# Kernel tuning notes

Measured on AMD Instinct MI355X. Metric: run time of the kernel, lower is better.

## Reference

```python
import jax, jax.numpy as jnp
import numpy as np

D_MODEL = 1024
NUM_HEADS = 16
D_K = D_MODEL // NUM_HEADS
B, T = 2, 2048


def setup_inputs() -> dict:
    key = jax.random.key(0)
    ks = jax.random.split(key, 9)
    s = 1.0 / np.sqrt(D_MODEL)
    inp = {"x": jax.random.normal(ks[0], (B, T, D_MODEL), dtype=jnp.float32)}
    for i, name in enumerate(["q", "k", "v", "out"]):
        inp[f"W_{name}"] = jax.random.uniform(ks[1 + 2 * i], (D_MODEL, D_MODEL), jnp.float32, -s, s)
        inp[f"b_{name}"] = jax.random.uniform(ks[2 + 2 * i], (D_MODEL,), jnp.float32, -s, s)
    return inp


def reference(x, W_q, b_q, W_k, b_k, W_v, b_v, W_out, b_out):
    b, t, _ = x.shape
    # torch Linear: y = x @ W.T + b
    def proj(inp, W, bias):
        y = inp @ W.T + bias
        return y.reshape(b, -1, NUM_HEADS, D_K).transpose(0, 2, 1, 3)  # [B,H,T,d_k]

    Q = proj(x, W_q, b_q)
    K = proj(x, W_k, b_k)
    V = proj(x, W_v, b_v)
    scores = jnp.einsum("bhqd,bhkd->bhqk", Q, K) / jnp.sqrt(jnp.float32(D_K))
    attn = jax.nn.softmax(scores, axis=-1)
    ctx = jnp.einsum("bhqk,bhkd->bhqd", attn, V)
    ctx = ctx.transpose(0, 2, 1, 3).reshape(b, t, D_MODEL)
    return ctx @ W_out.T + b_out
```

## Files before the change

### kernel.cpp

```cpp
#include <hip/hip_runtime.h>
#include <hip/hip_bf16.h>

typedef __attribute__((ext_vector_type(8))) short short8;
typedef __attribute__((ext_vector_type(4))) short short4v;
typedef __attribute__((ext_vector_type(4))) float floatx4;

__device__ __forceinline__ unsigned short f2b(float f) {
  unsigned int v;
  __builtin_memcpy(&v, &f, 4);
  unsigned int r = (v + 0x7FFFu + ((v >> 16) & 1u)) >> 16;
  return (unsigned short)r;
}

__device__ __forceinline__ unsigned int f2b_pk(float a, float b) {
  unsigned int ua, ub;
  __builtin_memcpy(&ua, &a, 4);
  __builtin_memcpy(&ub, &b, 4);
  ua = ua + 0x7FFFu + ((ua >> 16) & 1u);
  ub = ub + 0x7FFFu + ((ub >> 16) & 1u);
#if __has_builtin(__builtin_amdgcn_perm)
  return __builtin_amdgcn_perm(ub, ua, 0x07060302u);
#else
  return (ub & 0xFFFF0000u) | (ua >> 16);
#endif
}

__device__ __forceinline__ float fast_exp2(float x) {
#if __has_builtin(__builtin_amdgcn_exp2f)
  return __builtin_amdgcn_exp2f(x);
#else
  return __builtin_exp2f(x);
#endif
}

__device__ __forceinline__ void async_copy16(const void* g, void* l) {
  __builtin_amdgcn_global_load_lds(
      (const __attribute__((address_space(1))) unsigned int*)g,
      (__attribute__((address_space(3))) unsigned int*)l, 16, 0, 0);
}

#define QSCALE 0.18033688011112042f

__global__ __launch_bounds__(256) void cvt_all_kernel(
    const float* __restrict__ x,
    const float* __restrict__ w0, const float* __restrict__ w1,
    const float* __restrict__ w2, const float* __restrict__ w3,
    unsigned short* __restrict__ xb,
    unsigned short* __restrict__ d0, unsigned short* __restrict__ d1,
    unsigned short* __restrict__ d2, unsigned short* __restrict__ d3)
{
  int gid = blockIdx.x * 256 + threadIdx.x;
  const float* src;
  unsigned short* dst;
  size_t off;
  if (gid < (1 << 20)) {
    src = x; dst = xb; off = gid;
  } else {
    int g = gid - (1 << 20);
    int w = g >> 18;
    off = g & 0x3FFFF;
    src = (w == 0) ? w0 : (w == 1) ? w1 : (w == 2) ? w2 : w3;
    dst = (w == 0) ? d0 : (w == 1) ? d1 : (w == 2) ? d2 : d3;
  }
  floatx4 v = *(const floatx4*)(src + off * 4);
  unsigned int lo = f2b_pk(v[0], v[1]), hi = f2b_pk(v[2], v[3]);
  unsigned long long r = ((unsigned long long)hi << 32) | lo;
  *(unsigned long long*)(dst + off * 4) = r;
}

__global__ __launch_bounds__(256) void gemm_qkv_kernel(
    const unsigned short* __restrict__ A,
    const unsigned short* __restrict__ W0, const unsigned short* __restrict__ W1,
    const unsigned short* __restrict__ W2,
    const float* __restrict__ bias0, const float* __restrict__ bias1,
    const float* __restrict__ bias2,
    unsigned short* __restrict__ Qo, unsigned short* __restrict__ Ko,
    unsigned short* __restrict__ VTo)
{
  const int z = blockIdx.z;
  const unsigned short* W  = (z == 0) ? W0 : (z == 1) ? W1 : W2;
  const float* bias        = (z == 0) ? bias0 : (z == 1) ? bias1 : bias2;

  __shared__ alignas(16) unsigned short sA[128 * 32];
  __shared__ alignas(16) unsigned short sB[128 * 32];

  const int tid  = threadIdx.x;
  const int lane = tid & 63;
  const int wave = tid >> 6;
  const int col  = lane & 15;
  const int quad = lane >> 4;
  const int wm   = (wave >> 1) * 64;
  const int wn   = (wave & 1) * 64;
  const int m0   = blockIdx.y * 128;
  const int n0   = blockIdx.x * 128;
  const int swz8 = (quad ^ ((col >> 1) & 3)) * 8;

  floatx4 acc[4][4];
#pragma unroll
  for (int i = 0; i < 4; ++i)
#pragma unroll
    for (int j = 0; j < 4; ++j) acc[i][j] = (floatx4){0.f, 0.f, 0.f, 0.f};

  for (int k0 = 0; k0 < 1024; k0 += 32) {
    __syncthreads();
#pragma unroll
    for (int i = 0; i < 2; ++i) {
      int c   = i * 256 + tid;
      int row = c >> 2;
      int cs  = (c & 3) ^ ((c >> 3) & 3);
      int ko  = cs * 8;
      async_copy16(A + (size_t)(m0 + row) * 1024 + k0 + ko, sA + c * 8);
      async_copy16(W + (size_t)(n0 + row) * 1024 + k0 + ko, sB + c * 8);
    }
    __syncthreads();
    short8 af[4], bf[4];
#pragma unroll
    for (int mi = 0; mi < 4; ++mi)
      af[mi] = *(const short8*)(sA + (wm + mi * 16 + col) * 32 + swz8);
#pragma unroll
    for (int ni = 0; ni < 4; ++ni)
      bf[ni] = *(const short8*)(sB + (wn + ni * 16 + col) * 32 + swz8);
#pragma unroll
    for (int mi = 0; mi < 4; ++mi)
#pragma unroll
      for (int ni = 0; ni < 4; ++ni)
        acc[mi][ni] = __builtin_amdgcn_mfma_f32_16x16x32_bf16(af[mi], bf[ni], acc[mi][ni], 0, 0, 0);
  }

#pragma unroll
  for (int ni = 0; ni < 4; ++ni) {
    int n = n0 + wn + ni * 16 + col;
    float bv = bias[n];
#pragma unroll
    for (int mi = 0; mi < 4; ++mi) {
      int mbase = m0 + wm + mi * 16 + quad * 4;
      if (z == 2) {
        int d = n & 63, h = n >> 6;
        int bb = mbase >> 11, t = mbase & 2047;
        unsigned int lo = f2b_pk(acc[mi][ni][0] + bv, acc[mi][ni][1] + bv);
        unsigned int hi = f2b_pk(acc[mi][ni][2] + bv, acc[mi][ni][3] + bv);
        unsigned long long wv = ((unsigned long long)hi << 32) | lo;
        *(unsigned long long*)(VTo + (((size_t)bb * 16 + h) * 64 + d) * 2048 + t) = wv;
      } else {
#pragma unroll
        for (int r = 0; r < 4; ++r) {
          int m = mbase + r;
          float val = acc[mi][ni][r] + bv;
          if (z == 0) Qo[(size_t)m * 1024 + n] = f2b(val * QSCALE);
          else        Ko[(size_t)m * 1024 + n] = f2b(val);
        }
      }
    }
  }
}

__global__ __launch_bounds__(256) void gemm_out_kernel(
    const unsigned short* __restrict__ A, const unsigned short* __restrict__ W,
    const float* __restrict__ bias, float* __restrict__ DF)
{
  __shared__ alignas(16) unsigned short sA[128 * 32];
  __shared__ alignas(16) unsigned short sB[64 * 32];

  const int tid  = threadIdx.x;
  const int lane = tid & 63;
  const int wave = tid >> 6;
  const int col  = lane & 15;
  const int quad = lane >> 4;
  const int wm   = (wave >> 1) * 64;
  const int wn   = (wave & 1) * 32;
  const int m0   = blockIdx.y * 128;
  const int n0   = blockIdx.x * 64;
  const int swz8 = (quad ^ ((col >> 1) & 3)) * 8;

  floatx4 acc[4][2];
#pragma unroll
  for (int i = 0; i < 4; ++i)
#pragma unroll
    for (int j = 0; j < 2; ++j) acc[i][j] = (floatx4){0.f, 0.f, 0.f, 0.f};

  for (int k0 = 0; k0 < 1024; k0 += 32) {
    __syncthreads();
#pragma unroll
    for (int i = 0; i < 2; ++i) {
      int c   = i * 256 + tid;
      int row = c >> 2;
      int cs  = (c & 3) ^ ((c >> 3) & 3);
      async_copy16(A + (size_t)(m0 + row) * 1024 + k0 + cs * 8, sA + c * 8);
    }
    {
      int row = tid >> 2;
      int cs  = (tid & 3) ^ ((tid >> 3) & 3);
      async_copy16(W + (size_t)(n0 + row) * 1024 + k0 + cs * 8, sB + tid * 8);
    }
    __syncthreads();
    short8 af[4], bf[2];
#pragma unroll
    for (int mi = 0; mi < 4; ++mi)
      af[mi] = *(const short8*)(sA + (wm + mi * 16 + col) * 32 + swz8);
#pragma unroll
    for (int ni = 0; ni < 2; ++ni)
      bf[ni] = *(const short8*)(sB + (wn + ni * 16 + col) * 32 + swz8);
#pragma unroll
    for (int mi = 0; mi < 4; ++mi)
#pragma unroll
      for (int ni = 0; ni < 2; ++ni)
        acc[mi][ni] = __builtin_amdgcn_mfma_f32_16x16x32_bf16(af[mi], bf[ni], acc[mi][ni], 0, 0, 0);
  }

#pragma unroll
  for (int ni = 0; ni < 2; ++ni) {
    int n = n0 + wn + ni * 16 + col;
    float bv = bias[n];
#pragma unroll
    for (int mi = 0; mi < 4; ++mi) {
      int mbase = m0 + wm + mi * 16 + quad * 4;
#pragma unroll
      for (int r = 0; r < 4; ++r)
        DF[(size_t)(mbase + r) * 1024 + n] = acc[mi][ni][r] + bv;
    }
  }
}

__global__ __launch_bounds__(256, 2) void attention_kernel(
    const unsigned short* __restrict__ Q, const unsigned short* __restrict__ K,
    const unsigned short* __restrict__ VT, unsigned short* __restrict__ CTX)
{
  __shared__ alignas(16) unsigned short sK[2][8192];
  __shared__ alignas(16) unsigned short sV[2][8192];
  __shared__ alignas(16) unsigned short sP[4][32 * 64];

  const int flat = blockIdx.x;
  const int idx  = flat >> 3;
  const int bh   = (flat & 7) * 4 + (idx >> 4);
  const int q0   = (idx & 15) * 128;
  const int b = bh >> 4, h = bh & 15;

  const int tid  = threadIdx.x;
  const int lane = tid & 63;
  const int wave = tid >> 6;
  const int col  = lane & 15;
  const int quad = lane >> 4;
  const int c7   = col & 7;
  const int swz8 = (quad ^ ((col >> 1) & 3)) * 8;

  const int srow = tid >> 2;
  const int sko  = ((tid & 3) ^ ((tid >> 3) & 3)) * 8;

  const unsigned short* kbase = K + ((size_t)b * 2048 + srow) * 1024 + h * 64;
  const unsigned short* vbase = VT + ((size_t)bh * 64 + srow) * 2048;

  short8 qfA[2], qfB[2];
  {
    const unsigned short* qp =
        Q + ((size_t)(b * 2048 + q0 + wave * 32 + col)) * 1024 + h * 64 + quad * 8;
    qfA[0] = *(const short8*)qp;
    qfA[1] = *(const short8*)(qp + 32);
    qfB[0] = *(const short8*)(qp + 16 * 1024);
    qfB[1] = *(const short8*)(qp + 16 * 1024 + 32);
  }

#define STAGE_KV128(ktv, buf)                                                  \
  do {                                                                         \
    _Pragma("unroll")                                                          \
    for (int kh = 0; kh < 2; ++kh) {                                           \
      _Pragma("unroll")                                                        \
      for (int i = 0; i < 2; ++i) {                                            \
        async_copy16(kbase + (size_t)((ktv) + kh * 64) * 1024 + i * 32 + sko,  \
                     sK[buf] + kh * 4096 + (i * 256 + tid) * 8);               \
        async_copy16(vbase + (ktv) + kh * 64 + i * 32 + sko,                   \
                     sV[buf] + kh * 4096 + (i * 256 + tid) * 8);               \
      }                                                                        \
    }                                                                          \
  } while (0)

  STAGE_KV128(0, 0);

  floatx4 OA[4], OB[4];
#pragma unroll
  for (int f = 0; f < 4; ++f) {
    OA[f] = (floatx4){0.f, 0.f, 0.f, 0.f};
    OB[f] = (floatx4){0.f, 0.f, 0.f, 0.f};
  }
  float laccA = 0.f, laccB = 0.f;

  unsigned short* myP = &sP[wave][0];

  for (int kt = 0; kt < 2048; kt += 128) {
    const int cur = (kt >> 7) & 1;
    __syncthreads();
    if (kt + 128 < 2048) {
      STAGE_KV128(kt + 128, cur ^ 1);
    }

#pragma unroll
    for (int kh = 0; kh < 2; ++kh) {
      const unsigned short* sKc = sK[cur] + kh * 4096;
      const unsigned short* sVc = sV[cur] + kh * 4096;

      floatx4 STA[4], STB[4];
      __builtin_amdgcn_s_setprio(1);
#pragma unroll
      for (int f = 0; f < 4; ++f) {
        short8 kf0 = *(const short8*)(sKc + (f * 16 + col) * 32 + swz8);
        short8 kf1 = *(const short8*)(sKc + 2048 + (f * 16 + col) * 32 + swz8);
        STA[f] = (floatx4){0.f, 0.f, 0.f, 0.f};
        STA[f] = __builtin_amdgcn_mfma_f32_16x16x32_bf16(kf0, qfA[0], STA[f], 0, 0, 0);
        STA[f] = __builtin_amdgcn_mfma_f32_16x16x32_bf16(kf1, qfA[1], STA[f], 0, 0, 0);
        STB[f] = (floatx4){0.f, 0.f, 0.f, 0.f};
        STB[f] = __builtin_amdgcn_mfma_f32_16x16x32_bf16(kf0, qfB[0], STB[f], 0, 0, 0);
        STB[f] = __builtin_amdgcn_mfma_f32_16x16x32_bf16(kf1, qfB[1], STB[f], 0, 0, 0);
      }
      __builtin_amdgcn_s_setprio(0);

#pragma unroll
      for (int f = 0; f < 4; ++f) {
        float a0 = fast_exp2(STA[f][0]);
        float a1 = fast_exp2(STA[f][1]);
        float a2 = fast_exp2(STA[f][2]);
        float a3 = fast_exp2(STA[f][3]);
        laccA += (a0 + a1) + (a2 + a3);
        unsigned long long wA =
            ((unsigned long long)f2b_pk(a2, a3) << 32) | f2b_pk(a0, a1);
        *(unsigned long long*)(myP + col * 64 +
                               (((f * 2 + (quad >> 1)) ^ c7) * 8) + (quad & 1) * 4) = wA;
        float b0 = fast_exp2(STB[f][0]);
        float b1 = fast_exp2(STB[f][1]);
        float b2 = fast_exp2(STB[f][2]);
        float b3 = fast_exp2(STB[f][3]);
        laccB += (b0 + b1) + (b2 + b3);
        unsigned long long wB =
            ((unsigned long long)f2b_pk(b2, b3) << 32) | f2b_pk(b0, b1);
        *(unsigned long long*)(myP + (16 + col) * 64 +
                               (((f * 2 + (quad >> 1)) ^ c7) * 8) + (quad & 1) * 4) = wB;
      }

      short8 pfA0 = *(const short8*)(myP + col * 64 + ((quad ^ c7) * 8));
      short8 pfA1 = *(const short8*)(myP + col * 64 + (((quad + 4) ^ c7) * 8));
      short8 pfB0 = *(const short8*)(myP + (16 + col) * 64 + ((quad ^ c7) * 8));
      short8 pfB1 = *(const short8*)(myP + (16 + col) * 64 + (((quad + 4) ^ c7) * 8));
      __builtin_amdgcn_s_setprio(1);
#pragma unroll
      for (int f = 0; f < 4; ++f) {
        short8 vf0 = *(const short8*)(sVc + (f * 16 + col) * 32 + swz8);
        short8 vf1 = *(const short8*)(sVc + 2048 + (f * 16 + col) * 32 + swz8);
        OA[f] = __builtin_amdgcn_mfma_f32_16x16x32_bf16(pfA0, vf0, OA[f], 0, 0, 0);
        OA[f] = __builtin_amdgcn_mfma_f32_16x16x32_bf16(pfA1, vf1, OA[f], 0, 0, 0);
        OB[f] = __builtin_amdgcn_mfma_f32_16x16x32_bf16(pfB0, vf0, OB[f], 0, 0, 0);
        OB[f] = __builtin_amdgcn_mfma_f32_16x16x32_bf16(pfB1, vf1, OB[f], 0, 0, 0);
      }
      __builtin_amdgcn_s_setprio(0);
    }
  }

  laccA += __shfl_xor(laccA, 16, 64);
  laccA += __shfl_xor(laccA, 32, 64);
  laccB += __shfl_xor(laccB, 16, 64);
  laccB += __shfl_xor(laccB, 32, 64);
  float invA[4], invB[4];
#pragma unroll
  for (int r = 0; r < 4; ++r) {
    invA[r] = 1.f / __shfl(laccA, quad * 4 + r, 16);
    invB[r] = 1.f / __shfl(laccB, quad * 4 + r, 16);
  }

#pragma unroll
  for (int f = 0; f < 4; ++f) {
#pragma unroll
    for (int r = 0; r < 4; ++r) {
      int qA = q0 + wave * 32 + quad * 4 + r;
      int d = f * 16 + col;
      CTX[(size_t)(b * 2048 + qA) * 1024 + h * 64 + d] = f2b(OA[f][r] * invA[r]);
      CTX[(size_t)(b * 2048 + qA + 16) * 1024 + h * 64 + d] = f2b(OB[f][r] * invB[r]);
    }
  }
}

extern "C" void kernel_launch(void* const* d_in, const int* in_sizes, int n_in,
                              void* d_out, int out_size, void* d_ws, size_t ws_size,
                              hipStream_t stream) {
  const float* x   = (const float*)d_in[0];
  const float* W_q = (const float*)d_in[1];
  const float* b_q = (const float*)d_in[2];
  const float* W_k = (const float*)d_in[3];
  const float* b_k = (const float*)d_in[4];
  const float* W_v = (const float*)d_in[5];
  const float* b_v = (const float*)d_in[6];
  const float* W_o = (const float*)d_in[7];
  const float* b_o = (const float*)d_in[8];
  float* out = (float*)d_out;

  const size_t NX = (size_t)4096 * 1024;
  const size_t NW = (size_t)1024 * 1024;

  unsigned short* p   = (unsigned short*)d_ws;
  unsigned short* xb  = p;  p += NX;
  unsigned short* Wqb = p;  p += NW;
  unsigned short* Wkb = p;  p += NW;
  unsigned short* Wvb = p;  p += NW;
  unsigned short* Wob = p;  p += NW;
  unsigned short* Q   = p;  p += NX;
  unsigned short* Kb  = p;  p += NX;
  unsigned short* VT  = p;  p += NX;
  unsigned short* CTX = p;  p += NX;

  dim3 blk(256);
  cvt_all_kernel<<<dim3(8192), blk, 0, stream>>>(
      x, W_q, W_k, W_v, W_o, xb, Wqb, Wkb, Wvb, Wob);
  gemm_qkv_kernel<<<dim3(8, 32, 3), blk, 0, stream>>>(
      xb, Wqb, Wkb, Wvb, b_q, b_k, b_v, Q, Kb, VT);
  attention_kernel<<<dim3(512), blk, 0, stream>>>(Q, Kb, VT, CTX);
  gemm_out_kernel<<<dim3(16, 32), blk, 0, stream>>>(CTX, Wob, b_o, out);
}
```

Baseline: 192.7 us.

## Double per-wave query rows in attention to raise K/V tile reuse

Each attention block now handles 256 query rows instead of 128, with each wave processing 64 rows (four 16-row groups) against each staged K/V tile. This halves the number of blocks and the total K/V traffic from global to shared memory per query. The cost is higher register pressure (launch bounds dropped to one block per SM), a larger P scratch area in shared memory, and only 256 blocks on a 256-CU device, so there is less latency hiding.

```diff
diff --git a/kernel.cpp b/kernel.cpp
--- a/kernel.cpp
+++ b/kernel.cpp
@@ -221,18 +221,18 @@
   }
 }
 
-__global__ __launch_bounds__(256, 2) void attention_kernel(
+__global__ __launch_bounds__(256, 1) void attention_kernel(
     const unsigned short* __restrict__ Q, const unsigned short* __restrict__ K,
     const unsigned short* __restrict__ VT, unsigned short* __restrict__ CTX)
 {
   __shared__ alignas(16) unsigned short sK[2][8192];
   __shared__ alignas(16) unsigned short sV[2][8192];
-  __shared__ alignas(16) unsigned short sP[4][32 * 64];
+  __shared__ alignas(16) unsigned short sP[4][64 * 64];
 
   const int flat = blockIdx.x;
   const int idx  = flat >> 3;
-  const int bh   = (flat & 7) * 4 + (idx >> 4);
-  const int q0   = (idx & 15) * 128;
+  const int bh   = (flat & 7) * 4 + (idx >> 3);
+  const int q0   = (idx & 7) * 256;
   const int b = bh >> 4, h = bh & 15;
 
   const int tid  = threadIdx.x;
@@ -249,14 +249,15 @@
   const unsigned short* kbase = K + ((size_t)b * 2048 + srow) * 1024 + h * 64;
   const unsigned short* vbase = VT + ((size_t)bh * 64 + srow) * 2048;
 
-  short8 qfA[2], qfB[2];
+  short8 qf[4][2];
   {
     const unsigned short* qp =
-        Q + ((size_t)(b * 2048 + q0 + wave * 32 + col)) * 1024 + h * 64 + quad * 8;
-    qfA[0] = *(const short8*)qp;
-    qfA[1] = *(const short8*)(qp + 32);
-    qfB[0] = *(const short8*)(qp + 16 * 1024);
-    qfB[1] = *(const short8*)(qp + 16 * 1024 + 32);
+        Q + ((size_t)(b * 2048 + q0 + wave * 64 + col)) * 1024 + h * 64 + quad * 8;
+#pragma unroll
+    for (int g = 0; g < 4; ++g) {
+      qf[g][0] = *(const short8*)(qp + (size_t)g * 16 * 1024);
+      qf[g][1] = *(const short8*)(qp + (size_t)g * 16 * 1024 + 32);
+    }
   }
 
 #define STAGE_KV128(ktv, buf)                                                  \
@@ -275,13 +276,12 @@
 
   STAGE_KV128(0, 0);
 
-  floatx4 OA[4], OB[4];
-#pragma unroll
-  for (int f = 0; f < 4; ++f) {
-    OA[f] = (floatx4){0.f, 0.f, 0.f, 0.f};
-    OB[f] = (floatx4){0.f, 0.f, 0.f, 0.f};
-  }
-  float laccA = 0.f, laccB = 0.f;
+  floatx4 O[4][4];
+#pragma unroll
+  for (int g = 0; g < 4; ++g)
+#pragma unroll
+    for (int f = 0; f < 4; ++f) O[g][f] = (floatx4){0.f, 0.f, 0.f, 0.f};
+  float lacc[4] = {0.f, 0.f, 0.f, 0.f};
 
   unsigned short* myP = &sP[wave][0];
 
@@ -297,80 +297,80 @@
       const unsigned short* sKc = sK[cur] + kh * 4096;
       const unsigned short* sVc = sV[cur] + kh * 4096;
 
-      floatx4 STA[4], STB[4];
+      floatx4 ST[4][4];
       __builtin_amdgcn_s_setprio(1);
 #pragma unroll
       for (int f = 0; f < 4; ++f) {
         short8 kf0 = *(const short8*)(sKc + (f * 16 + col) * 32 + swz8);
         short8 kf1 = *(const short8*)(sKc + 2048 + (f * 16 + col) * 32 + swz8);
-        STA[f] = (floatx4){0.f, 0.f, 0.f, 0.f};
-        STA[f] = __builtin_amdgcn_mfma_f32_16x16x32_bf16(kf0, qfA[0], STA[f], 0, 0, 0);
-        STA[f] = __builtin_amdgcn_mfma_f32_16x16x32_bf16(kf1, qfA[1], STA[f], 0, 0, 0);
-        STB[f] = (floatx4){0.f, 0.f, 0.f, 0.f};
-        STB[f] = __builtin_amdgcn_mfma_f32_16x16x32_bf16(kf0, qfB[0], STB[f], 0, 0, 0);
-        STB[f] = __builtin_amdgcn_mfma_f32_16x16x32_bf16(kf1, qfB[1], STB[f], 0, 0, 0);
+#pragma unroll
+        for (int g = 0; g < 4; ++g) {
+          ST[g][f] = (floatx4){0.f, 0.f, 0.f, 0.f};
+          ST[g][f] = __builtin_amdgcn_mfma_f32_16x16x32_bf16(kf0, qf[g][0], ST[g][f], 0, 0, 0);
+          ST[g][f] = __builtin_amdgcn_mfma_f32_16x16x32_bf16(kf1, qf[g][1], ST[g][f], 0, 0, 0);
+        }
       }
       __builtin_amdgcn_s_setprio(0);
 
 #pragma unroll
-      for (int f = 0; f < 4; ++f) {
-        float a0 = fast_exp2(STA[f][0]);
-        float a1 = fast_exp2(STA[f][1]);
-        float a2 = fast_exp2(STA[f][2]);
-        float a3 = fast_exp2(STA[f][3]);
-        laccA += (a0 + a1) + (a2 + a3);
-        unsigned long long wA =
-            ((unsigned long long)f2b_pk(a2, a3) << 32) | f2b_pk(a0, a1);
-        *(unsigned long long*)(myP + col * 64 +
-                               (((f * 2 + (quad >> 1)) ^ c7) * 8) + (quad & 1) * 4) = wA;
-        float b0 = fast_exp2(STB[f][0]);
-        float b1 = fast_exp2(STB[f][1]);
-        float b2 = fast_exp2(STB[f][2]);
-        float b3 = fast_exp2(STB[f][3]);
-        laccB += (b0 + b1) + (b2 + b3);
-        unsigned long long wB =
-            ((unsigned long long)f2b_pk(b2, b3) << 32) | f2b_pk(b0, b1);
-        *(unsigned long long*)(myP + (16 + col) * 64 +
-                               (((f * 2 + (quad >> 1)) ^ c7) * 8) + (quad & 1) * 4) = wB;
-      }
-
-      short8 pfA0 = *(const short8*)(myP + col * 64 + ((quad ^ c7) * 8));
-      short8 pfA1 = *(const short8*)(myP + col * 64 + (((quad + 4) ^ c7) * 8));
-      short8 pfB0 = *(const short8*)(myP + (16 + col) * 64 + ((quad ^ c7) * 8));
-      short8 pfB1 = *(const short8*)(myP + (16 + col) * 64 + (((quad + 4) ^ c7) * 8));
+      for (int g = 0; g < 4; ++g) {
+#pragma unroll
+        for (int f = 0; f < 4; ++f) {
+          float p0 = fast_exp2(ST[g][f][0]);
+          float p1 = fast_exp2(ST[g][f][1]);
+          float p2 = fast_exp2(ST[g][f][2]);
+          float p3 = fast_exp2(ST[g][f][3]);
+          lacc[g] += (p0 + p1) + (p2 + p3);
+          unsigned long long w =
+              ((unsigned long long)f2b_pk(p2, p3) << 32) | f2b_pk(p0, p1);
+          *(unsigned long long*)(myP + (g * 16 + col) * 64 +
+                                 (((f * 2 + (quad >> 1)) ^ c7) * 8) + (quad & 1) * 4) = w;
+        }
+      }
+
+      short8 pf[4][2];
+#pragma unroll
+      for (int g = 0; g < 4; ++g) {
+        pf[g][0] = *(const short8*)(myP + (g * 16 + col) * 64 + ((quad ^ c7) * 8));
+        pf[g][1] = *(const short8*)(myP + (g * 16 + col) * 64 + (((quad + 4) ^ c7) * 8));
+      }
       __builtin_amdgcn_s_setprio(1);
 #pragma unroll
       for (int f = 0; f < 4; ++f) {
         short8 vf0 = *(const short8*)(sVc + (f * 16 + col) * 32 + swz8);
         short8 vf1 = *(const short8*)(sVc + 2048 + (f * 16 + col) * 32 + swz8);
-        OA[f] = __builtin_amdgcn_mfma_f32_16x16x32_bf16(pfA0, vf0, OA[f], 0, 0, 0);
-        OA[f] = __builtin_amdgcn_mfma_f32_16x16x32_bf16(pfA1, vf1, OA[f], 0, 0, 0);
-        OB[f] = __builtin_amdgcn_mfma_f32_16x16x32_bf16(pfB0, vf0, OB[f], 0, 0, 0);
-        OB[f] = __builtin_amdgcn_mfma_f32_16x16x32_bf16(pfB1, vf1, OB[f], 0, 0, 0);
+#pragma unroll
+        for (int g = 0; g < 4; ++g) {
+          O[g][f] = __builtin_amdgcn_mfma_f32_16x16x32_bf16(pf[g][0], vf0, O[g][f], 0, 0, 0);
+          O[g][f] = __builtin_amdgcn_mfma_f32_16x16x32_bf16(pf[g][1], vf1, O[g][f], 0, 0, 0);
+        }
       }
       __builtin_amdgcn_s_setprio(0);
     }
   }
 
-  laccA += __shfl_xor(laccA, 16, 64);
-  laccA += __shfl_xor(laccA, 32, 64);
-  laccB += __shfl_xor(laccB, 16, 64);
-  laccB += __shfl_xor(laccB, 32, 64);
-  float invA[4], invB[4];
-#pragma unroll
-  for (int r = 0; r < 4; ++r) {
-    invA[r] = 1.f / __shfl(laccA, quad * 4 + r, 16);
-    invB[r] = 1.f / __shfl(laccB, quad * 4 + r, 16);
-  }
-
-#pragma unroll
-  for (int f = 0; f < 4; ++f) {
-#pragma unroll
-    for (int r = 0; r < 4; ++r) {
-      int qA = q0 + wave * 32 + quad * 4 + r;
-      int d = f * 16 + col;
-      CTX[(size_t)(b * 2048 + qA) * 1024 + h * 64 + d] = f2b(OA[f][r] * invA[r]);
-      CTX[(size_t)(b * 2048 + qA + 16) * 1024 + h * 64 + d] = f2b(OB[f][r] * invB[r]);
+#pragma unroll
+  for (int g = 0; g < 4; ++g) {
+    lacc[g] += __shfl_xor(lacc[g], 16, 64);
+    lacc[g] += __shfl_xor(lacc[g], 32, 64);
+  }
+  float inv[4][4];
+#pragma unroll
+  for (int g = 0; g < 4; ++g)
+#pragma unroll
+    for (int r = 0; r < 4; ++r)
+      inv[g][r] = 1.f / __shfl(lacc[g], quad * 4 + r, 16);
+
+#pragma unroll
+  for (int g = 0; g < 4; ++g) {
+#pragma unroll
+    for (int f = 0; f < 4; ++f) {
+#pragma unroll
+      for (int r = 0; r < 4; ++r) {
+        int q = q0 + wave * 64 + g * 16 + quad * 4 + r;
+        int d = f * 16 + col;
+        CTX[(size_t)(b * 2048 + q) * 1024 + h * 64 + d] = f2b(O[g][f][r] * inv[g][r]);
+      }
     }
   }
 }
@@ -408,6 +408,6 @@
       x, W_q, W_k, W_v, W_o, xb, Wqb, Wkb, Wvb, Wob);
   gemm_qkv_kernel<<<dim3(8, 32, 3), blk, 0, stream>>>(
       xb, Wqb, Wkb, Wvb, b_q, b_k, b_v, Q, Kb, VT);
-  attention_kernel<<<dim3(512), blk, 0, stream>>>(Q, Kb, VT, CTX);
+  attention_kernel<<<dim3(256), blk, 0, stream>>>(Q, Kb, VT, CTX);
   gemm_out_kernel<<<dim3(16, 32), blk, 0, stream>>>(CTX, Wob, b_o, out);
 }
```

Measured after the change: 209.5 us. 8.8% more time.

## Software-pipeline PV MFMAs one step behind the QK^T MFMAs

Applied to the files above, without the earlier changes.

Restructures the attention inner loop so the P·V MFMAs for the previous 64-key half-tile run right after the current QK^T MFMAs. The P and V fragments are loaded into registers at the end of each step and consumed in the next one, with an epilogue after the loop. The aim is to overlap the exp/bf16 pack/LDS round-trip of P with matrix work and keep the MFMA pipe busy. The cost is more live registers (P and V fragments held across steps), which could lower occupancy or cause spills. The V fragments are read before the next __syncthreads, so the double-buffer reuse stays safe.

```diff
diff --git a/kernel.cpp b/kernel.cpp
--- a/kernel.cpp
+++ b/kernel.cpp
@@ -285,6 +285,9 @@
 
   unsigned short* myP = &sP[wave][0];
 
+  short8 pfA0p, pfA1p, pfB0p, pfB1p;
+  short8 vfp[4][2];
+
   for (int kt = 0; kt < 2048; kt += 128) {
     const int cur = (kt >> 7) & 1;
     __syncthreads();
@@ -309,6 +312,16 @@
         STB[f] = (floatx4){0.f, 0.f, 0.f, 0.f};
         STB[f] = __builtin_amdgcn_mfma_f32_16x16x32_bf16(kf0, qfB[0], STB[f], 0, 0, 0);
         STB[f] = __builtin_amdgcn_mfma_f32_16x16x32_bf16(kf1, qfB[1], STB[f], 0, 0, 0);
+      }
+
+      if (kt != 0 || kh != 0) {
+#pragma unroll
+        for (int f = 0; f < 4; ++f) {
+          OA[f] = __builtin_amdgcn_mfma_f32_16x16x32_bf16(pfA0p, vfp[f][0], OA[f], 0, 0, 0);
+          OA[f] = __builtin_amdgcn_mfma_f32_16x16x32_bf16(pfA1p, vfp[f][1], OA[f], 0, 0, 0);
+          OB[f] = __builtin_amdgcn_mfma_f32_16x16x32_bf16(pfB0p, vfp[f][0], OB[f], 0, 0, 0);
+          OB[f] = __builtin_amdgcn_mfma_f32_16x16x32_bf16(pfB1p, vfp[f][1], OB[f], 0, 0, 0);
+        }
       }
       __builtin_amdgcn_s_setprio(0);
 
@@ -334,22 +347,24 @@
                                (((f * 2 + (quad >> 1)) ^ c7) * 8) + (quad & 1) * 4) = wB;
       }
 
-      short8 pfA0 = *(const short8*)(myP + col * 64 + ((quad ^ c7) * 8));
-      short8 pfA1 = *(const short8*)(myP + col * 64 + (((quad + 4) ^ c7) * 8));
-      short8 pfB0 = *(const short8*)(myP + (16 + col) * 64 + ((quad ^ c7) * 8));
-      short8 pfB1 = *(const short8*)(myP + (16 + col) * 64 + (((quad + 4) ^ c7) * 8));
-      __builtin_amdgcn_s_setprio(1);
+      pfA0p = *(const short8*)(myP + col * 64 + ((quad ^ c7) * 8));
+      pfA1p = *(const short8*)(myP + col * 64 + (((quad + 4) ^ c7) * 8));
+      pfB0p = *(const short8*)(myP + (16 + col) * 64 + ((quad ^ c7) * 8));
+      pfB1p = *(const short8*)(myP + (16 + col) * 64 + (((quad + 4) ^ c7) * 8));
 #pragma unroll
       for (int f = 0; f < 4; ++f) {
-        short8 vf0 = *(const short8*)(sVc + (f * 16 + col) * 32 + swz8);
-        short8 vf1 = *(const short8*)(sVc + 2048 + (f * 16 + col) * 32 + swz8);
-        OA[f] = __builtin_amdgcn_mfma_f32_16x16x32_bf16(pfA0, vf0, OA[f], 0, 0, 0);
-        OA[f] = __builtin_amdgcn_mfma_f32_16x16x32_bf16(pfA1, vf1, OA[f], 0, 0, 0);
-        OB[f] = __builtin_amdgcn_mfma_f32_16x16x32_bf16(pfB0, vf0, OB[f], 0, 0, 0);
-        OB[f] = __builtin_amdgcn_mfma_f32_16x16x32_bf16(pfB1, vf1, OB[f], 0, 0, 0);
+        vfp[f][0] = *(const short8*)(sVc + (f * 16 + col) * 32 + swz8);
+        vfp[f][1] = *(const short8*)(sVc + 2048 + (f * 16 + col) * 32 + swz8);
       }
-      __builtin_amdgcn_s_setprio(0);
-    }
+    }
+  }
+
+#pragma unroll
+  for (int f = 0; f < 4; ++f) {
+    OA[f] = __builtin_amdgcn_mfma_f32_16x16x32_bf16(pfA0p, vfp[f][0], OA[f], 0, 0, 0);
+    OA[f] = __builtin_amdgcn_mfma_f32_16x16x32_bf16(pfA1p, vfp[f][1], OA[f], 0, 0, 0);
+    OB[f] = __builtin_amdgcn_mfma_f32_16x16x32_bf16(pfB0p, vfp[f][0], OB[f], 0, 0, 0);
+    OB[f] = __builtin_amdgcn_mfma_f32_16x16x32_bf16(pfB1p, vfp[f][1], OB[f], 0, 0, 0);
   }
 
   laccA += __shfl_xor(laccA, 16, 64);
```

Result: no change. 194.1 us (+0.8%).
